# Optimization experiments

Measured on AMD Instinct MI355X. Metric: run time of the kernel, lower is better.

## Reference

```python
import jax, jax.numpy as jnp
import numpy as np

BLOCK_SIZE = 64
SPARSITY_RATIO = 0.5


def _band_mask(seq_len, block_size, sparsity_ratio):
    # Block (i, j) is computed iff max(0, i-w) <= j < min(nb, i+w), w = int(nb*ratio).
    nb = seq_len // block_size
    w = int(nb * sparsity_ratio)
    ib = jnp.arange(nb)
    bm = (ib[None, :] >= ib[:, None] - w) & (ib[None, :] < ib[:, None] + w)  # [nb, nb]
    return jnp.repeat(jnp.repeat(bm, block_size, axis=0), block_size, axis=1)  # [S, S]


def setup_inputs() -> dict:
    key = jax.random.key(0)
    kq, kk, kv = jax.random.split(key, 3)
    B, S, D = 4, 4096, 128
    return {
        "query": jax.random.normal(kq, (B, S, D), dtype=jnp.float32),
        "key": jax.random.normal(kk, (B, S, D), dtype=jnp.float32),
        "value": jax.random.normal(kv, (B, S, D), dtype=jnp.float32),
    }


def reference(query, key, value):
    B, S, D = query.shape
    mask = _band_mask(S, BLOCK_SIZE, SPARSITY_RATIO)  # [S, S] bool
    scores = jnp.einsum('bqd,bkd->bqk', query, key)  # [B, S, S]
    # Outside-band entries stay exactly 0 (NOT -inf) — matches torch.zeros init.
    scores = jnp.where(mask[None, :, :], scores, jnp.zeros((), scores.dtype))
    probs = jax.nn.softmax(scores, axis=-1)
    return jnp.matmul(probs, value)  # [B, S, D]
```

## Files before the change

### kernel.cpp

```cpp
#include <hip/hip_runtime.h>


typedef _Float16 f16;
typedef __attribute__((ext_vector_type(8))) _Float16 f16x8;
typedef __attribute__((ext_vector_type(4))) _Float16 f16x4;
typedef __attribute__((ext_vector_type(4))) float f32x4;

#define MFMA16(a, b, c) __builtin_amdgcn_mfma_f32_16x16x32_f16((a), (b), (c), 0, 0, 0)

#define BATCH 4
#define SEQ   4096
#define DIM   128
#define NB    64
#define WBAND 32
#define LOG2E 1.44269504088896f
#define DTHR  8.0f

#define KTILE 16384
#define VTILE 16384
#define TSTR  72

#define CHUNKS 8
#define PART_STRIDE 16896

__device__ __forceinline__ void gl16(const char* g, char* l) {
  __builtin_amdgcn_global_load_lds(
      (const __attribute__((address_space(1))) void*)g,
      (__attribute__((address_space(3))) void*)l, 16, 0, 0);
}

__global__ __launch_bounds__(256) void convert_kernel(
    const float* __restrict__ K, const float* __restrict__ V,
    f16* __restrict__ KT, f16* __restrict__ VT, float* __restrict__ BS) {
  __shared__ f16 T[128 * TSTR];
  const int blk = blockIdx.x;
  const int b = blk >> 6, jb = blk & 63;
  const int s0 = jb * 64;
  const int t = threadIdx.x;
  char* ktile = (char*)KT + (size_t)blk * KTILE;
  char* vtile = (char*)VT + (size_t)blk * VTILE;

#pragma unroll
  for (int i = 0; i < 4; ++i) {
    int idx = t + i * 256;
    int row = idx >> 4;
    int c = idx & 15;
    const float* src = K + ((size_t)(b * SEQ + s0 + row)) * DIM + c * 8;
    float4 a = *(const float4*)src;
    float4 d = *(const float4*)(src + 4);
    f16x8 h = {(f16)a.x, (f16)a.y, (f16)a.z, (f16)a.w,
               (f16)d.x, (f16)d.y, (f16)d.z, (f16)d.w};
    *(f16x8*)(ktile + row * 256 + ((c ^ (row & 15)) * 16)) = h;
  }

#pragma unroll
  for (int i = 0; i < 8; ++i) {
    int idx = t + i * 256;
    int row = idx >> 5;
    int c4 = (idx & 31) * 4;
    float4 v = *(const float4*)(V + (size_t)(b * SEQ + s0 + row) * DIM + c4);
    T[(c4 + 0) * TSTR + row] = (f16)v.x;
    T[(c4 + 1) * TSTR + row] = (f16)v.y;
    T[(c4 + 2) * TSTR + row] = (f16)v.z;
    T[(c4 + 3) * TSTR + row] = (f16)v.w;
  }
  __syncthreads();

#pragma unroll
  for (int i = 0; i < 4; ++i) {
    int idx = t + i * 256;
    int d = idx >> 3;
    int c = idx & 7;
    f16x8 val = *(const f16x8*)(T + d * TSTR + c * 8);
    *(f16x8*)(vtile + d * 128 + ((c ^ (d & 7)) * 16)) = val;
  }

  if (t < 128) {
    float s = 0.f;
    for (int k = 0; k < 64; ++k) s += (float)T[t * TSTR + k];
    BS[(b * NB + jb) * DIM + t] = s;
  }
}

__global__ __launch_bounds__(256, 3) void attn_kernel(
    const float* __restrict__ Q, const f16* __restrict__ KT,
    const f16* __restrict__ VT, char* __restrict__ PART) {
  __shared__ __align__(16) char smem[49152];

  const int id = blockIdx.x;
  const int lin = (id & 7) * 128 + (id >> 3);
  const int ck = lin & 7;
  const int pair = lin >> 3;
  const int b = pair >> 5, p = pair & 31;

  const int t = threadIdx.x;
  const int w = t >> 6, l = t & 63, lg = l >> 4, ll = l & 15;
  const int half = w >> 1, qh = w & 1;
  const int myib = p * 2 + half;

  const int jloU = max(0, p * 2 - WBAND);
  const int jhiU = min(NB, p * 2 + 1 + WBAND);
  const int lenU = jhiU - jloU;
  const int c = (lenU + CHUNKS - 1) >> 3;
  const int j0 = jloU + ck * c;
  const int nloc = min(c, jhiU - j0);
  const int mylo = max(0, myib - WBAND);
  const int myhi = min(NB, myib + WBAND);

  f16x8 qf[2][4];
#pragma unroll
  for (int s = 0; s < 2; ++s) {
    const float* qrow =
        Q + ((size_t)(b * SEQ + myib * 64 + qh * 32 + s * 16 + ll)) * DIM;
#pragma unroll
    for (int ks = 0; ks < 4; ++ks) {
      int d0 = ks * 32 + lg * 8;
      float4 a = *(const float4*)(qrow + d0);
      float4 cc = *(const float4*)(qrow + d0 + 4);
      float vv[8] = {a.x, a.y, a.z, a.w, cc.x, cc.y, cc.z, cc.w};
#pragma unroll
      for (int e = 0; e < 8; ++e) qf[s][ks][e] = (f16)(vv[e] * LOG2E);
    }
  }

  float m2[2] = {0.f, 0.f};
  float ell[2] = {0.f, 0.f};
  f32x4 o[2][8];
#pragma unroll
  for (int s = 0; s < 2; ++s)
#pragma unroll
    for (int nt = 0; nt < 8; ++nt) o[s][nt] = (f32x4){0.f, 0.f, 0.f, 0.f};

  f16* Pw = (f16*)(smem + 32768 + w * 4096);
  const char* kb = smem;
  const char* vb = smem + 16384;

  auto stage = [&](int jb) {
    const char* kg = (const char*)KT + ((size_t)(b * NB + jb)) * KTILE + t * 16;
    const char* vg = (const char*)VT + ((size_t)(b * NB + jb)) * VTILE + t * 16;
#pragma unroll
    for (int i = 0; i < 4; ++i) gl16(kg + i * 4096, smem + t * 16 + i * 4096);
#pragma unroll
    for (int i = 0; i < 4; ++i) gl16(vg + i * 4096, smem + 16384 + t * 16 + i * 4096);
  };

  if (nloc > 0) {
    stage(j0);
    __syncthreads();

    for (int tt = 0; tt < nloc; ++tt) {
      const int j = j0 + tt;
      const bool act = (j >= mylo) && (j < myhi);
      if (act) {
        f32x4 sacc[2][4];
#pragma unroll
        for (int s = 0; s < 2; ++s)
#pragma unroll
          for (int jt = 0; jt < 4; ++jt) sacc[s][jt] = (f32x4){0.f, 0.f, 0.f, 0.f};
        __builtin_amdgcn_s_setprio(1);
#pragma unroll
        for (int ks = 0; ks < 4; ++ks) {
#pragma unroll
          for (int jt = 0; jt < 4; ++jt) {
            int row = jt * 16 + ll;
            f16x8 kf = *(const f16x8*)(kb + row * 256 + (((ks * 4 + lg) ^ ll) * 16));
            sacc[0][jt] = MFMA16(kf, qf[0][ks], sacc[0][jt]);
            sacc[1][jt] = MFMA16(kf, qf[1][ks], sacc[1][jt]);
          }
        }
        __builtin_amdgcn_s_setprio(0);

#pragma unroll
        for (int s = 0; s < 2; ++s) {
          float vm = sacc[s][0][0];
#pragma unroll
          for (int jt = 0; jt < 4; ++jt)
#pragma unroll
            for (int r = 0; r < 4; ++r) vm = fmaxf(vm, sacc[s][jt][r]);
          vm = fmaxf(vm, __shfl_xor(vm, 16));
          vm = fmaxf(vm, __shfl_xor(vm, 32));

          if (__any(vm - m2[s] > DTHR)) {
            float nm = fmaxf(m2[s], vm);
            float scl = __builtin_amdgcn_exp2f(m2[s] - nm);
            m2[s] = nm;
            ell[s] *= scl;
            float sb[4];
#pragma unroll
            for (int r = 0; r < 4; ++r) sb[r] = __shfl(scl, lg * 4 + r);
#pragma unroll
            for (int nt = 0; nt < 8; ++nt)
#pragma unroll
              for (int r = 0; r < 4; ++r) o[s][nt][r] *= sb[r];
          }

          float rsum = 0.f;
#pragma unroll
          for (int jt = 0; jt < 4; ++jt) {
            f16x4 pk;
#pragma unroll
            for (int r = 0; r < 4; ++r) {
              float pv = __builtin_amdgcn_exp2f(sacc[s][jt][r] - m2[s]);
              rsum += pv;
              pk[r] = (f16)pv;
            }
            *(f16x4*)(Pw + s * 1024 + ll * 64 +
                      ((jt * 16 + lg * 4) ^ ((ll & 7) << 3))) = pk;
          }
          ell[s] += rsum;
        }

        __builtin_amdgcn_s_setprio(1);
#pragma unroll
        for (int ks2 = 0; ks2 < 2; ++ks2) {
          int pcol = (ks2 * 32 + lg * 8) ^ ((ll & 7) << 3);
          f16x8 pa0 = *(const f16x8*)(Pw + ll * 64 + pcol);
          f16x8 pa1 = *(const f16x8*)(Pw + 1024 + ll * 64 + pcol);
#pragma unroll
          for (int nt = 0; nt < 8; ++nt) {
            int d = nt * 16 + ll;
            f16x8 vbf = *(const f16x8*)(vb + d * 128 + (((ks2 * 4 + lg) ^ (ll & 7)) * 16));
            o[0][nt] = MFMA16(pa0, vbf, o[0][nt]);
            o[1][nt] = MFMA16(pa1, vbf, o[1][nt]);
          }
        }
        __builtin_amdgcn_s_setprio(0);
      }
      __syncthreads();
      if (tt + 1 < nloc) stage(j0 + tt + 1);
      __syncthreads();
    }
  }

#pragma unroll
  for (int s = 0; s < 2; ++s) {
    ell[s] += __shfl_xor(ell[s], 16);
    ell[s] += __shfl_xor(ell[s], 32);
  }

  char* pb = PART + ((size_t)((pair * CHUNKS + ck) * 2 + half)) * PART_STRIDE;
#pragma unroll
  for (int s = 0; s < 2; ++s)
#pragma unroll
    for (int g = 0; g < 4; ++g) {
      f16x8 hh;
#pragma unroll
      for (int r = 0; r < 4; ++r) {
        hh[r] = (f16)o[s][2 * g][r];
        hh[4 + r] = (f16)o[s][2 * g + 1][r];
      }
      *(f16x8*)(pb + qh * 8192 + ((s * 4 + g) * 64 + l) * 16) = hh;
    }
  if (lg == 0) {
#pragma unroll
    for (int s = 0; s < 2; ++s)
      *(float2*)(pb + 16384 + (qh * 32 + s * 16 + ll) * 8) =
          make_float2(m2[s], ell[s]);
  }
}

__global__ __launch_bounds__(256) void merge_kernel(
    const char* __restrict__ PART, const float* __restrict__ BS,
    float* __restrict__ Out) {
  __shared__ float VoutS[DIM];
  __shared__ float mlS[CHUNKS][64][2];

  const int id = blockIdx.x;
  const int lin = (id & 7) * 32 + (id >> 3);
  const int pair = lin >> 1, half = lin & 1;
  const int b = pair >> 5;
  const int ib = (pair & 31) * 2 + half;
  const int t = threadIdx.x;
  const int l = t & 63, lg = (t >> 4) & 3, ll = t & 15;
  const int sub = (t >> 6) & 1, qh = t >> 7;

  const int jlo = max(0, ib - WBAND);
  const int jhi = min(NB, ib + WBAND);
  const float cnt_out = (float)(SEQ - (jhi - jlo) * 64);

  if (t < DIM) {
    float s = 0.f;
    for (int j = 0; j < jlo; ++j) s += BS[(b * NB + j) * DIM + t];
    for (int j = jhi; j < NB; ++j) s += BS[(b * NB + j) * DIM + t];
    VoutS[t] = s;
  }

  const size_t pb0 = ((size_t)(pair * CHUNKS * 2 + half)) * PART_STRIDE;
  for (int i = t; i < CHUNKS * 64; i += 256) {
    int k = i >> 6, row = i & 63;
    *(float2*)&mlS[k][row][0] = *(const float2*)(
        PART + pb0 + (size_t)k * 2 * PART_STRIDE + 16384 + row * 8);
  }
  __syncthreads();

  float aw[4][CHUNKS], en[4], inv[4];
#pragma unroll
  for (int r = 0; r < 4; ++r) {
    int row = qh * 32 + sub * 16 + lg * 4 + r;
    float M = mlS[0][row][0];
#pragma unroll
    for (int k = 1; k < CHUNKS; ++k) M = fmaxf(M, mlS[k][row][0]);
    en[r] = __builtin_amdgcn_exp2f(-M);
    float den = cnt_out * en[r];
#pragma unroll
    for (int k = 0; k < CHUNKS; ++k) {
      aw[r][k] = __builtin_amdgcn_exp2f(mlS[k][row][0] - M);
      den += aw[r][k] * mlS[k][row][1];
    }
    inv[r] = 1.f / den;
  }

  float acc[8][4];
#pragma unroll
  for (int nt = 0; nt < 8; ++nt)
#pragma unroll
    for (int r = 0; r < 4; ++r) acc[nt][r] = 0.f;

  for (int k = 0; k < CHUNKS; ++k) {
    const char* oc = PART + pb0 + (size_t)k * 2 * PART_STRIDE + qh * 8192;
#pragma unroll
    for (int g = 0; g < 4; ++g) {
      f16x8 h = *(const f16x8*)(oc + ((sub * 4 + g) * 64 + l) * 16);
#pragma unroll
      for (int r = 0; r < 4; ++r) {
        acc[2 * g][r] += aw[r][k] * (float)h[r];
        acc[2 * g + 1][r] += aw[r][k] * (float)h[4 + r];
      }
    }
  }

  const int q0 = ib * 64;
#pragma unroll
  for (int nt = 0; nt < 8; ++nt) {
    int col = nt * 16 + ll;
    float vout = VoutS[col];
#pragma unroll
    for (int r = 0; r < 4; ++r) {
      int row = qh * 32 + sub * 16 + lg * 4 + r;
      Out[((size_t)(b * SEQ + q0 + row)) * DIM + col] =
          (acc[nt][r] + en[r] * vout) * inv[r];
    }
  }
}

extern "C" void kernel_launch(void* const* d_in, const int* in_sizes, int n_in,
                              void* d_out, int out_size, void* d_ws, size_t ws_size,
                              hipStream_t stream) {
  const float* Q = (const float*)d_in[0];
  const float* K = (const float*)d_in[1];
  const float* V = (const float*)d_in[2];
  float* Out = (float*)d_out;

  char* ws = (char*)d_ws;
  f16* KTg = (f16*)ws;
  f16* VTg = (f16*)(ws + (size_t)BATCH * NB * KTILE);
  float* BS = (float*)(ws + 2 * (size_t)BATCH * NB * KTILE);
  char* PART = ws + 2 * (size_t)BATCH * NB * KTILE + (size_t)BATCH * NB * DIM * 4;

  convert_kernel<<<dim3(BATCH * NB), 256, 0, stream>>>(K, V, KTg, VTg, BS);
  attn_kernel<<<dim3(BATCH * NB / 2 * CHUNKS), 256, 0, stream>>>(Q, KTg, VTg, PART);
  merge_kernel<<<dim3(BATCH * NB), 256, 0, stream>>>(PART, BS, Out);
}
```

Baseline: 65.14 us.

## Pre-swizzle K/V/Q into MFMA fragment layout and drop LDS staging in attention

The convert kernel now writes K, V and a LOG2E-scaled fp16 copy of Q directly in per-lane MFMA fragment order. The attention kernel then loads operands straight from global memory with coalesced 16-byte loads, and it no longer stages K/V tiles through shared memory with block barriers. P now stays in registers instead of going through an LDS round trip. Each wave independently owns a chunk of one query block, which removes the inactive-tile waste from the old pair scheme. The cost is that every wave re-reads K/V from global/L2 with no intra-block sharing, and Q conversion moves into the prep kernel.

```diff
diff --git a/kernel.cpp b/kernel.cpp
--- a/kernel.cpp
+++ b/kernel.cpp
@@ -15,43 +15,22 @@
 #define WBAND 32
 #define LOG2E 1.44269504088896f
 #define DTHR  8.0f
-
-#define KTILE 16384
-#define VTILE 16384
 #define TSTR  72
 
+#define TILE  16384
+#define QTILE 8192
 #define CHUNKS 8
 #define PART_STRIDE 16896
 
-__device__ __forceinline__ void gl16(const char* g, char* l) {
-  __builtin_amdgcn_global_load_lds(
-      (const __attribute__((address_space(1))) void*)g,
-      (__attribute__((address_space(3))) void*)l, 16, 0, 0);
-}
-
 __global__ __launch_bounds__(256) void convert_kernel(
-    const float* __restrict__ K, const float* __restrict__ V,
-    f16* __restrict__ KT, f16* __restrict__ VT, float* __restrict__ BS) {
+    const float* __restrict__ Q, const float* __restrict__ K,
+    const float* __restrict__ V, f16* __restrict__ KF, f16* __restrict__ VF,
+    f16* __restrict__ QF, float* __restrict__ BS) {
   __shared__ f16 T[128 * TSTR];
   const int blk = blockIdx.x;
   const int b = blk >> 6, jb = blk & 63;
   const int s0 = jb * 64;
   const int t = threadIdx.x;
-  char* ktile = (char*)KT + (size_t)blk * KTILE;
-  char* vtile = (char*)VT + (size_t)blk * VTILE;
-
-#pragma unroll
-  for (int i = 0; i < 4; ++i) {
-    int idx = t + i * 256;
-    int row = idx >> 4;
-    int c = idx & 15;
-    const float* src = K + ((size_t)(b * SEQ + s0 + row)) * DIM + c * 8;
-    float4 a = *(const float4*)src;
-    float4 d = *(const float4*)(src + 4);
-    f16x8 h = {(f16)a.x, (f16)a.y, (f16)a.z, (f16)a.w,
-               (f16)d.x, (f16)d.y, (f16)d.z, (f16)d.w};
-    *(f16x8*)(ktile + row * 256 + ((c ^ (row & 15)) * 16)) = h;
-  }
 
 #pragma unroll
   for (int i = 0; i < 8; ++i) {
@@ -64,15 +43,53 @@
     T[(c4 + 2) * TSTR + row] = (f16)v.z;
     T[(c4 + 3) * TSTR + row] = (f16)v.w;
   }
-  __syncthreads();
-
+
+  char* kt = (char*)KF + (size_t)blk * TILE;
 #pragma unroll
   for (int i = 0; i < 4; ++i) {
     int idx = t + i * 256;
-    int d = idx >> 3;
-    int c = idx & 7;
-    f16x8 val = *(const f16x8*)(T + d * TSTR + c * 8);
-    *(f16x8*)(vtile + d * 128 + ((c ^ (d & 7)) * 16)) = val;
+    int frag = idx >> 6, lane = idx & 63;
+    int ks = frag >> 2, jt = frag & 3;
+    int row = jt * 16 + (lane & 15);
+    int d0 = ks * 32 + (lane >> 4) * 8;
+    const float* src = K + ((size_t)(b * SEQ + s0 + row)) * DIM + d0;
+    float4 a = *(const float4*)src;
+    float4 d = *(const float4*)(src + 4);
+    f16x8 h = {(f16)a.x, (f16)a.y, (f16)a.z, (f16)a.w,
+               (f16)d.x, (f16)d.y, (f16)d.z, (f16)d.w};
+    *(f16x8*)(kt + idx * 16) = h;
+  }
+
+  char* qt = (char*)QF + (size_t)blk * (2 * QTILE);
+#pragma unroll
+  for (int i = 0; i < 4; ++i) {
+    int idx = t + i * 256;
+    int qh = idx >> 9, frag = (idx >> 6) & 7, lane = idx & 63;
+    int s = frag >> 2, ks = frag & 3;
+    int row = qh * 32 + s * 16 + (lane & 15);
+    int d0 = ks * 32 + (lane >> 4) * 8;
+    const float* src = Q + ((size_t)(b * SEQ + s0 + row)) * DIM + d0;
+    float4 a = *(const float4*)src;
+    float4 d = *(const float4*)(src + 4);
+    f16x8 h = {(f16)(a.x * LOG2E), (f16)(a.y * LOG2E), (f16)(a.z * LOG2E),
+               (f16)(a.w * LOG2E), (f16)(d.x * LOG2E), (f16)(d.y * LOG2E),
+               (f16)(d.z * LOG2E), (f16)(d.w * LOG2E)};
+    *(f16x8*)(qt + idx * 16) = h;
+  }
+  __syncthreads();
+
+  char* vt = (char*)VF + (size_t)blk * TILE;
+#pragma unroll
+  for (int i = 0; i < 4; ++i) {
+    int idx = t + i * 256;
+    int frag = idx >> 6, lane = idx & 63;
+    int ks2 = frag >> 3, nt = frag & 7;
+    int d = nt * 16 + (lane & 15);
+    int k0 = ks2 * 32 + ((lane >> 4) & 3) * 4;
+    f16x4 x = *(const f16x4*)(T + d * TSTR + k0);
+    f16x4 y = *(const f16x4*)(T + d * TSTR + k0 + 16);
+    f16x8 h = {x[0], x[1], x[2], x[3], y[0], y[1], y[2], y[3]};
+    *(f16x8*)(vt + idx * 16) = h;
   }
 
   if (t < 128) {
@@ -83,45 +100,34 @@
 }
 
 __global__ __launch_bounds__(256, 3) void attn_kernel(
-    const float* __restrict__ Q, const f16* __restrict__ KT,
-    const f16* __restrict__ VT, char* __restrict__ PART) {
-  __shared__ __align__(16) char smem[49152];
-
+    const f16* __restrict__ KF, const f16* __restrict__ VF,
+    const f16* __restrict__ QF, char* __restrict__ PART) {
   const int id = blockIdx.x;
-  const int lin = (id & 7) * 128 + (id >> 3);
-  const int ck = lin & 7;
-  const int pair = lin >> 3;
-  const int b = pair >> 5, p = pair & 31;
-
   const int t = threadIdx.x;
   const int w = t >> 6, l = t & 63, lg = l >> 4, ll = l & 15;
-  const int half = w >> 1, qh = w & 1;
-  const int myib = p * 2 + half;
-
-  const int jloU = max(0, p * 2 - WBAND);
-  const int jhiU = min(NB, p * 2 + 1 + WBAND);
-  const int lenU = jhiU - jloU;
-  const int c = (lenU + CHUNKS - 1) >> 3;
-  const int j0 = jloU + ck * c;
-  const int nloc = min(c, jhiU - j0);
-  const int mylo = max(0, myib - WBAND);
-  const int myhi = min(NB, myib + WBAND);
-
+
+  const int lin = (id & 7) * 128 + (id >> 3);
+  const int b = lin >> 8;
+  const int ib = (lin >> 2) & 63;
+  const int ckp = lin & 3;
+  const int ck = ckp * 2 + (w >> 1);
+  const int qh = w & 1;
+
+  const int jlo = max(0, ib - WBAND);
+  const int jhi = min(NB, ib + WBAND);
+  const int n = jhi - jlo;
+  const int c = (n + 7) >> 3;
+  const int j0 = jlo + ck * c;
+  const int nloc = min(c, jhi - j0);
+
+  const char* qt = (const char*)QF +
+                   ((size_t)((b * NB + ib) * 2 + qh)) * QTILE + (size_t)l * 16;
   f16x8 qf[2][4];
 #pragma unroll
-  for (int s = 0; s < 2; ++s) {
-    const float* qrow =
-        Q + ((size_t)(b * SEQ + myib * 64 + qh * 32 + s * 16 + ll)) * DIM;
-#pragma unroll
-    for (int ks = 0; ks < 4; ++ks) {
-      int d0 = ks * 32 + lg * 8;
-      float4 a = *(const float4*)(qrow + d0);
-      float4 cc = *(const float4*)(qrow + d0 + 4);
-      float vv[8] = {a.x, a.y, a.z, a.w, cc.x, cc.y, cc.z, cc.w};
-#pragma unroll
-      for (int e = 0; e < 8; ++e) qf[s][ks][e] = (f16)(vv[e] * LOG2E);
-    }
-  }
+  for (int s = 0; s < 2; ++s)
+#pragma unroll
+    for (int ks = 0; ks < 4; ++ks)
+      qf[s][ks] = *(const f16x8*)(qt + (s * 4 + ks) * 1024);
 
   float m2[2] = {0.f, 0.f};
   float ell[2] = {0.f, 0.f};
@@ -131,105 +137,85 @@
 #pragma unroll
     for (int nt = 0; nt < 8; ++nt) o[s][nt] = (f32x4){0.f, 0.f, 0.f, 0.f};
 
-  f16* Pw = (f16*)(smem + 32768 + w * 4096);
-  const char* kb = smem;
-  const char* vb = smem + 16384;
-
-  auto stage = [&](int jb) {
-    const char* kg = (const char*)KT + ((size_t)(b * NB + jb)) * KTILE + t * 16;
-    const char* vg = (const char*)VT + ((size_t)(b * NB + jb)) * VTILE + t * 16;
-#pragma unroll
-    for (int i = 0; i < 4; ++i) gl16(kg + i * 4096, smem + t * 16 + i * 4096);
-#pragma unroll
-    for (int i = 0; i < 4; ++i) gl16(vg + i * 4096, smem + 16384 + t * 16 + i * 4096);
-  };
-
-  if (nloc > 0) {
-    stage(j0);
-    __syncthreads();
-
-    for (int tt = 0; tt < nloc; ++tt) {
-      const int j = j0 + tt;
-      const bool act = (j >= mylo) && (j < myhi);
-      if (act) {
-        f32x4 sacc[2][4];
-#pragma unroll
-        for (int s = 0; s < 2; ++s)
-#pragma unroll
-          for (int jt = 0; jt < 4; ++jt) sacc[s][jt] = (f32x4){0.f, 0.f, 0.f, 0.f};
-        __builtin_amdgcn_s_setprio(1);
-#pragma unroll
-        for (int ks = 0; ks < 4; ++ks) {
-#pragma unroll
-          for (int jt = 0; jt < 4; ++jt) {
-            int row = jt * 16 + ll;
-            f16x8 kf = *(const f16x8*)(kb + row * 256 + (((ks * 4 + lg) ^ ll) * 16));
-            sacc[0][jt] = MFMA16(kf, qf[0][ks], sacc[0][jt]);
-            sacc[1][jt] = MFMA16(kf, qf[1][ks], sacc[1][jt]);
+  const char* kt = (const char*)KF + ((size_t)(b * NB + j0)) * TILE + (size_t)l * 16;
+  const char* vt = (const char*)VF + ((size_t)(b * NB + j0)) * TILE + (size_t)l * 16;
+
+  for (int tt = 0; tt < nloc; ++tt) {
+    f32x4 sacc[2][4];
+#pragma unroll
+    for (int s = 0; s < 2; ++s)
+#pragma unroll
+      for (int jt = 0; jt < 4; ++jt) sacc[s][jt] = (f32x4){0.f, 0.f, 0.f, 0.f};
+
+    __builtin_amdgcn_s_setprio(1);
+#pragma unroll
+    for (int ks = 0; ks < 4; ++ks) {
+#pragma unroll
+      for (int jt = 0; jt < 4; ++jt) {
+        f16x8 kf = *(const f16x8*)(kt + (ks * 4 + jt) * 1024);
+        sacc[0][jt] = MFMA16(kf, qf[0][ks], sacc[0][jt]);
+        sacc[1][jt] = MFMA16(kf, qf[1][ks], sacc[1][jt]);
+      }
+    }
+    __builtin_amdgcn_s_setprio(0);
+
+    f16x8 pa[2][2];
+#pragma unroll
+    for (int s = 0; s < 2; ++s) {
+      float vm = sacc[s][0][0];
+#pragma unroll
+      for (int jt = 0; jt < 4; ++jt)
+#pragma unroll
+        for (int r = 0; r < 4; ++r) vm = fmaxf(vm, sacc[s][jt][r]);
+      vm = fmaxf(vm, __shfl_xor(vm, 16));
+      vm = fmaxf(vm, __shfl_xor(vm, 32));
+
+      if (__any(vm - m2[s] > DTHR)) {
+        float nm = fmaxf(m2[s], vm);
+        float scl = __builtin_amdgcn_exp2f(m2[s] - nm);
+        m2[s] = nm;
+        ell[s] *= scl;
+        float sb[4];
+#pragma unroll
+        for (int r = 0; r < 4; ++r) sb[r] = __shfl(scl, lg * 4 + r);
+#pragma unroll
+        for (int nt = 0; nt < 8; ++nt)
+#pragma unroll
+          for (int r = 0; r < 4; ++r) o[s][nt][r] *= sb[r];
+      }
+
+      float rsum = 0.f;
+#pragma unroll
+      for (int ks2 = 0; ks2 < 2; ++ks2) {
+        f16x8 pv;
+#pragma unroll
+        for (int u = 0; u < 2; ++u) {
+#pragma unroll
+          for (int r = 0; r < 4; ++r) {
+            float p = __builtin_amdgcn_exp2f(sacc[s][ks2 * 2 + u][r] - m2[s]);
+            rsum += p;
+            pv[u * 4 + r] = (f16)p;
           }
         }
-        __builtin_amdgcn_s_setprio(0);
-
-#pragma unroll
-        for (int s = 0; s < 2; ++s) {
-          float vm = sacc[s][0][0];
-#pragma unroll
-          for (int jt = 0; jt < 4; ++jt)
-#pragma unroll
-            for (int r = 0; r < 4; ++r) vm = fmaxf(vm, sacc[s][jt][r]);
-          vm = fmaxf(vm, __shfl_xor(vm, 16));
-          vm = fmaxf(vm, __shfl_xor(vm, 32));
-
-          if (__any(vm - m2[s] > DTHR)) {
-            float nm = fmaxf(m2[s], vm);
-            float scl = __builtin_amdgcn_exp2f(m2[s] - nm);
-            m2[s] = nm;
-            ell[s] *= scl;
-            float sb[4];
-#pragma unroll
-            for (int r = 0; r < 4; ++r) sb[r] = __shfl(scl, lg * 4 + r);
-#pragma unroll
-            for (int nt = 0; nt < 8; ++nt)
-#pragma unroll
-              for (int r = 0; r < 4; ++r) o[s][nt][r] *= sb[r];
-          }
-
-          float rsum = 0.f;
-#pragma unroll
-          for (int jt = 0; jt < 4; ++jt) {
-            f16x4 pk;
-#pragma unroll
-            for (int r = 0; r < 4; ++r) {
-              float pv = __builtin_amdgcn_exp2f(sacc[s][jt][r] - m2[s]);
-              rsum += pv;
-              pk[r] = (f16)pv;
-            }
-            *(f16x4*)(Pw + s * 1024 + ll * 64 +
-                      ((jt * 16 + lg * 4) ^ ((ll & 7) << 3))) = pk;
-          }
-          ell[s] += rsum;
-        }
-
-        __builtin_amdgcn_s_setprio(1);
-#pragma unroll
-        for (int ks2 = 0; ks2 < 2; ++ks2) {
-          int pcol = (ks2 * 32 + lg * 8) ^ ((ll & 7) << 3);
-          f16x8 pa0 = *(const f16x8*)(Pw + ll * 64 + pcol);
-          f16x8 pa1 = *(const f16x8*)(Pw + 1024 + ll * 64 + pcol);
-#pragma unroll
-          for (int nt = 0; nt < 8; ++nt) {
-            int d = nt * 16 + ll;
-            f16x8 vbf = *(const f16x8*)(vb + d * 128 + (((ks2 * 4 + lg) ^ (ll & 7)) * 16));
-            o[0][nt] = MFMA16(pa0, vbf, o[0][nt]);
-            o[1][nt] = MFMA16(pa1, vbf, o[1][nt]);
-          }
-        }
-        __builtin_amdgcn_s_setprio(0);
-      }
-      __syncthreads();
-      if (tt + 1 < nloc) stage(j0 + tt + 1);
-      __syncthreads();
-    }
+        pa[s][ks2] = pv;
+      }
+      ell[s] += rsum;
+    }
+
+    __builtin_amdgcn_s_setprio(1);
+#pragma unroll
+    for (int ks2 = 0; ks2 < 2; ++ks2) {
+#pragma unroll
+      for (int nt = 0; nt < 8; ++nt) {
+        f16x8 vbf = *(const f16x8*)(vt + (ks2 * 8 + nt) * 1024);
+        o[0][nt] = MFMA16(pa[0][ks2], vbf, o[0][nt]);
+        o[1][nt] = MFMA16(pa[1][ks2], vbf, o[1][nt]);
+      }
+    }
+    __builtin_amdgcn_s_setprio(0);
+
+    kt += TILE;
+    vt += TILE;
   }
 
 #pragma unroll
@@ -238,6 +224,8 @@
     ell[s] += __shfl_xor(ell[s], 32);
   }
 
+  const int pair = b * 32 + (ib >> 1);
+  const int half = ib & 1;
   char* pb = PART + ((size_t)((pair * CHUNKS + ck) * 2 + half)) * PART_STRIDE;
 #pragma unroll
   for (int s = 0; s < 2; ++s)
@@ -352,12 +340,13 @@
   float* Out = (float*)d_out;
 
   char* ws = (char*)d_ws;
-  f16* KTg = (f16*)ws;
-  f16* VTg = (f16*)(ws + (size_t)BATCH * NB * KTILE);
-  float* BS = (float*)(ws + 2 * (size_t)BATCH * NB * KTILE);
-  char* PART = ws + 2 * (size_t)BATCH * NB * KTILE + (size_t)BATCH * NB * DIM * 4;
-
-  convert_kernel<<<dim3(BATCH * NB), 256, 0, stream>>>(K, V, KTg, VTg, BS);
-  attn_kernel<<<dim3(BATCH * NB / 2 * CHUNKS), 256, 0, stream>>>(Q, KTg, VTg, PART);
+  f16* KF = (f16*)ws;
+  f16* VF = (f16*)(ws + (size_t)BATCH * NB * TILE);
+  f16* QF = (f16*)(ws + 2 * (size_t)BATCH * NB * TILE);
+  float* BS = (float*)(ws + 3 * (size_t)BATCH * NB * TILE);
+  char* PART = ws + 3 * (size_t)BATCH * NB * TILE + (size_t)BATCH * NB * DIM * 4;
+
+  convert_kernel<<<dim3(BATCH * NB), 256, 0, stream>>>(Q, K, V, KF, VF, QF, BS);
+  attn_kernel<<<dim3(BATCH * NB / 2 * CHUNKS), 256, 0, stream>>>(KF, VF, QF, PART);
   merge_kernel<<<dim3(BATCH * NB), 256, 0, stream>>>(PART, BS, Out);
 }
```

Result: slower. 90.47 us (+38.9%).

## Pre-pack K/V into MFMA fragment order, double-buffer tiles, keep P in registers

Applied to the files above, without the earlier changes.

The convert kernel now writes K and V tiles in the exact per-lane MFMA fragment order, so the attention kernel reads each operand with one linear 16-byte LDS load and no swizzle math. The attention kernel double-buffers K/V tiles in 64KB of LDS with async global-to-LDS loads and vmcnt waits, which lets the next tile's fetch overlap compute. P stays in registers because the exp2 output layout already matches the PV MFMA A operand, which removes the per-wave P LDS round trip. The cost is lower occupancy (2 blocks instead of 3) and reliance on hand-placed waitcnt and barrier ordering.

```diff
diff --git a/kernel.cpp b/kernel.cpp
--- a/kernel.cpp
+++ b/kernel.cpp
@@ -15,11 +15,9 @@
 #define WBAND 32
 #define LOG2E 1.44269504088896f
 #define DTHR  8.0f
-
-#define KTILE 16384
-#define VTILE 16384
 #define TSTR  72
 
+#define TILE  16384
 #define CHUNKS 8
 #define PART_STRIDE 16896
 
@@ -31,27 +29,12 @@
 
 __global__ __launch_bounds__(256) void convert_kernel(
     const float* __restrict__ K, const float* __restrict__ V,
-    f16* __restrict__ KT, f16* __restrict__ VT, float* __restrict__ BS) {
+    f16* __restrict__ KF, f16* __restrict__ VF, float* __restrict__ BS) {
   __shared__ f16 T[128 * TSTR];
   const int blk = blockIdx.x;
   const int b = blk >> 6, jb = blk & 63;
   const int s0 = jb * 64;
   const int t = threadIdx.x;
-  char* ktile = (char*)KT + (size_t)blk * KTILE;
-  char* vtile = (char*)VT + (size_t)blk * VTILE;
-
-#pragma unroll
-  for (int i = 0; i < 4; ++i) {
-    int idx = t + i * 256;
-    int row = idx >> 4;
-    int c = idx & 15;
-    const float* src = K + ((size_t)(b * SEQ + s0 + row)) * DIM + c * 8;
-    float4 a = *(const float4*)src;
-    float4 d = *(const float4*)(src + 4);
-    f16x8 h = {(f16)a.x, (f16)a.y, (f16)a.z, (f16)a.w,
-               (f16)d.x, (f16)d.y, (f16)d.z, (f16)d.w};
-    *(f16x8*)(ktile + row * 256 + ((c ^ (row & 15)) * 16)) = h;
-  }
 
 #pragma unroll
   for (int i = 0; i < 8; ++i) {
@@ -64,15 +47,36 @@
     T[(c4 + 2) * TSTR + row] = (f16)v.z;
     T[(c4 + 3) * TSTR + row] = (f16)v.w;
   }
-  __syncthreads();
-
+
+  char* kt = (char*)KF + (size_t)blk * TILE;
 #pragma unroll
   for (int i = 0; i < 4; ++i) {
     int idx = t + i * 256;
-    int d = idx >> 3;
-    int c = idx & 7;
-    f16x8 val = *(const f16x8*)(T + d * TSTR + c * 8);
-    *(f16x8*)(vtile + d * 128 + ((c ^ (d & 7)) * 16)) = val;
+    int frag = idx >> 6, lane = idx & 63;
+    int ks = frag >> 2, jt = frag & 3;
+    int row = jt * 16 + (lane & 15);
+    int d0 = ks * 32 + (lane >> 4) * 8;
+    const float* src = K + ((size_t)(b * SEQ + s0 + row)) * DIM + d0;
+    float4 a = *(const float4*)src;
+    float4 d = *(const float4*)(src + 4);
+    f16x8 h = {(f16)a.x, (f16)a.y, (f16)a.z, (f16)a.w,
+               (f16)d.x, (f16)d.y, (f16)d.z, (f16)d.w};
+    *(f16x8*)(kt + idx * 16) = h;
+  }
+  __syncthreads();
+
+  char* vt = (char*)VF + (size_t)blk * TILE;
+#pragma unroll
+  for (int i = 0; i < 4; ++i) {
+    int idx = t + i * 256;
+    int frag = idx >> 6, lane = idx & 63;
+    int ks2 = frag >> 3, nt = frag & 7;
+    int d = nt * 16 + (lane & 15);
+    int k0 = ks2 * 32 + ((lane >> 4) & 3) * 4;
+    f16x4 x = *(const f16x4*)(T + d * TSTR + k0);
+    f16x4 y = *(const f16x4*)(T + d * TSTR + k0 + 16);
+    f16x8 h = {x[0], x[1], x[2], x[3], y[0], y[1], y[2], y[3]};
+    *(f16x8*)(vt + idx * 16) = h;
   }
 
   if (t < 128) {
@@ -82,10 +86,10 @@
   }
 }
 
-__global__ __launch_bounds__(256, 3) void attn_kernel(
-    const float* __restrict__ Q, const f16* __restrict__ KT,
-    const f16* __restrict__ VT, char* __restrict__ PART) {
-  __shared__ __align__(16) char smem[49152];
+__global__ __launch_bounds__(256, 2) void attn_kernel(
+    const float* __restrict__ Q, const f16* __restrict__ KF,
+    const f16* __restrict__ VF, char* __restrict__ PART) {
+  __shared__ __align__(16) char smem[65536];
 
   const int id = blockIdx.x;
   const int lin = (id & 7) * 128 + (id >> 3);
@@ -122,6 +126,7 @@
       for (int e = 0; e < 8; ++e) qf[s][ks][e] = (f16)(vv[e] * LOG2E);
     }
   }
+  asm volatile("s_waitcnt vmcnt(0)" ::: "memory");
 
   float m2[2] = {0.f, 0.f};
   float ell[2] = {0.f, 0.f};
@@ -131,45 +136,53 @@
 #pragma unroll
     for (int nt = 0; nt < 8; ++nt) o[s][nt] = (f32x4){0.f, 0.f, 0.f, 0.f};
 
-  f16* Pw = (f16*)(smem + 32768 + w * 4096);
-  const char* kb = smem;
-  const char* vb = smem + 16384;
-
-  auto stage = [&](int jb) {
-    const char* kg = (const char*)KT + ((size_t)(b * NB + jb)) * KTILE + t * 16;
-    const char* vg = (const char*)VT + ((size_t)(b * NB + jb)) * VTILE + t * 16;
-#pragma unroll
-    for (int i = 0; i < 4; ++i) gl16(kg + i * 4096, smem + t * 16 + i * 4096);
-#pragma unroll
-    for (int i = 0; i < 4; ++i) gl16(vg + i * 4096, smem + 16384 + t * 16 + i * 4096);
+  auto stage = [&](int buf, int jb) {
+    const char* kg = (const char*)KF + ((size_t)(b * NB + jb)) * TILE + t * 16;
+    const char* vg = (const char*)VF + ((size_t)(b * NB + jb)) * TILE + t * 16;
+    char* kl = smem + buf * 32768 + t * 16;
+#pragma unroll
+    for (int i = 0; i < 4; ++i) gl16(kg + i * 4096, kl + i * 4096);
+#pragma unroll
+    for (int i = 0; i < 4; ++i) gl16(vg + i * 4096, kl + 16384 + i * 4096);
   };
 
   if (nloc > 0) {
-    stage(j0);
-    __syncthreads();
+    stage(0, j0);
+    if (nloc > 1) stage(1, j0 + 1);
 
     for (int tt = 0; tt < nloc; ++tt) {
+      if (tt + 1 < nloc) {
+        asm volatile("s_waitcnt vmcnt(8)" ::: "memory");
+      } else {
+        asm volatile("s_waitcnt vmcnt(0)" ::: "memory");
+      }
+      __builtin_amdgcn_s_barrier();
+      __builtin_amdgcn_sched_barrier(0);
+
       const int j = j0 + tt;
-      const bool act = (j >= mylo) && (j < myhi);
-      if (act) {
+      const char* kb = smem + (tt & 1) * 32768;
+      const char* vb = kb + 16384;
+
+      if (j >= mylo && j < myhi) {
         f32x4 sacc[2][4];
 #pragma unroll
         for (int s = 0; s < 2; ++s)
 #pragma unroll
           for (int jt = 0; jt < 4; ++jt) sacc[s][jt] = (f32x4){0.f, 0.f, 0.f, 0.f};
+
         __builtin_amdgcn_s_setprio(1);
 #pragma unroll
         for (int ks = 0; ks < 4; ++ks) {
 #pragma unroll
           for (int jt = 0; jt < 4; ++jt) {
-            int row = jt * 16 + ll;
-            f16x8 kf = *(const f16x8*)(kb + row * 256 + (((ks * 4 + lg) ^ ll) * 16));
+            f16x8 kf = *(const f16x8*)(kb + (ks * 4 + jt) * 1024 + l * 16);
             sacc[0][jt] = MFMA16(kf, qf[0][ks], sacc[0][jt]);
             sacc[1][jt] = MFMA16(kf, qf[1][ks], sacc[1][jt]);
           }
         }
         __builtin_amdgcn_s_setprio(0);
 
+        f16x8 pa[2][2];
 #pragma unroll
         for (int s = 0; s < 2; ++s) {
           float vm = sacc[s][0][0];
@@ -196,16 +209,18 @@
 
           float rsum = 0.f;
 #pragma unroll
-          for (int jt = 0; jt < 4; ++jt) {
-            f16x4 pk;
-#pragma unroll
-            for (int r = 0; r < 4; ++r) {
-              float pv = __builtin_amdgcn_exp2f(sacc[s][jt][r] - m2[s]);
-              rsum += pv;
-              pk[r] = (f16)pv;
+          for (int ks2 = 0; ks2 < 2; ++ks2) {
+            f16x8 pv;
+#pragma unroll
+            for (int u = 0; u < 2; ++u) {
+#pragma unroll
+              for (int r = 0; r < 4; ++r) {
+                float pe = __builtin_amdgcn_exp2f(sacc[s][ks2 * 2 + u][r] - m2[s]);
+                rsum += pe;
+                pv[u * 4 + r] = (f16)pe;
+              }
             }
-            *(f16x4*)(Pw + s * 1024 + ll * 64 +
-                      ((jt * 16 + lg * 4) ^ ((ll & 7) << 3))) = pk;
+            pa[s][ks2] = pv;
           }
           ell[s] += rsum;
         }
@@ -213,22 +228,18 @@
         __builtin_amdgcn_s_setprio(1);
 #pragma unroll
         for (int ks2 = 0; ks2 < 2; ++ks2) {
-          int pcol = (ks2 * 32 + lg * 8) ^ ((ll & 7) << 3);
-          f16x8 pa0 = *(const f16x8*)(Pw + ll * 64 + pcol);
-          f16x8 pa1 = *(const f16x8*)(Pw + 1024 + ll * 64 + pcol);
 #pragma unroll
           for (int nt = 0; nt < 8; ++nt) {
-            int d = nt * 16 + ll;
-            f16x8 vbf = *(const f16x8*)(vb + d * 128 + (((ks2 * 4 + lg) ^ (ll & 7)) * 16));
-            o[0][nt] = MFMA16(pa0, vbf, o[0][nt]);
-            o[1][nt] = MFMA16(pa1, vbf, o[1][nt]);
+            f16x8 vbf = *(const f16x8*)(vb + (ks2 * 8 + nt) * 1024 + l * 16);
+            o[0][nt] = MFMA16(pa[0][ks2], vbf, o[0][nt]);
+            o[1][nt] = MFMA16(pa[1][ks2], vbf, o[1][nt]);
           }
         }
         __builtin_amdgcn_s_setprio(0);
       }
-      __syncthreads();
-      if (tt + 1 < nloc) stage(j0 + tt + 1);
-      __syncthreads();
+
+      __builtin_amdgcn_s_barrier();
+      if (tt + 2 < nloc) stage(tt & 1, j0 + tt + 2);
     }
   }
 
@@ -352,12 +363,12 @@
   float* Out = (float*)d_out;
 
   char* ws = (char*)d_ws;
-  f16* KTg = (f16*)ws;
-  f16* VTg = (f16*)(ws + (size_t)BATCH * NB * KTILE);
-  float* BS = (float*)(ws + 2 * (size_t)BATCH * NB * KTILE);
-  char* PART = ws + 2 * (size_t)BATCH * NB * KTILE + (size_t)BATCH * NB * DIM * 4;
-
-  convert_kernel<<<dim3(BATCH * NB), 256, 0, stream>>>(K, V, KTg, VTg, BS);
-  attn_kernel<<<dim3(BATCH * NB / 2 * CHUNKS), 256, 0, stream>>>(Q, KTg, VTg, PART);
+  f16* KF = (f16*)ws;
+  f16* VF = (f16*)(ws + (size_t)BATCH * NB * TILE);
+  float* BS = (float*)(ws + 2 * (size_t)BATCH * NB * TILE);
+  char* PART = ws + 2 * (size_t)BATCH * NB * TILE + (size_t)BATCH * NB * DIM * 4;
+
+  convert_kernel<<<dim3(BATCH * NB), 256, 0, stream>>>(K, V, KF, VF, BS);
+  attn_kernel<<<dim3(BATCH * NB / 2 * CHUNKS), 256, 0, stream>>>(Q, KF, VF, PART);
   merge_kernel<<<dim3(BATCH * NB), 256, 0, stream>>>(PART, BS, Out);
 }
```

Measured after the change: 66.22 us. About the same (+1.7%).
